# Kernel tuning notes

Hardware: AMD Instinct MI355X
Metric: run time of the kernel (lower is better)

Reference implementation:

```python
import jax, jax.numpy as jnp
import numpy as np

N, M, D, C = 8192, 4096, 512, 100


def mish(x):
    return x * jnp.tanh(jax.nn.softplus(x))


def encode_dml(x, W1, b1, W2, b2):
    # two Linear(d_in, d_in) layers each followed by Mish
    h = mish(x @ W1 + b1)
    return mish(h @ W2 + b2)


def setup_inputs() -> dict:
    key = jax.random.key(0)
    ks = jax.random.split(key, 8)
    s = 1.0 / np.sqrt(D)
    x = jax.random.normal(ks[0], (N, D), dtype=jnp.float32)
    samples = jax.random.normal(ks[1], (M, D), dtype=jnp.float32)
    W1 = jax.random.normal(ks[2], (D, D), dtype=jnp.float32) * s
    b1 = jnp.zeros((D,), dtype=jnp.float32)
    W2 = jax.random.normal(ks[3], (D, D), dtype=jnp.float32) * s
    b2 = jnp.zeros((D,), dtype=jnp.float32)
    Wp = jax.random.normal(ks[4], (M, C), dtype=jnp.float32) * (1.0 / np.sqrt(M))
    bp = jnp.zeros((C,), dtype=jnp.float32)
    return {"x": x, "samples": samples, "W1": W1, "b1": b1,
            "W2": W2, "b2": b2, "Wp": Wp, "bp": bp}


def reference(x, samples, W1, b1, W2, b2, Wp, bp):
    xe = encode_dml(x, W1, b1, W2, b2)        # [N, D]
    se = encode_dml(samples, W1, b1, W2, b2)  # [M, D]
    # Euclidean distance to every anchor, GEMM-trick form of
    # torch.norm(x[:,None,:] - s[None,:,:], dim=-1)
    d2 = (jnp.sum(xe * xe, axis=1)[:, None]
          + jnp.sum(se * se, axis=1)[None, :]
          - 2.0 * (xe @ se.T))                # [N, M]
    dist = jnp.sqrt(jnp.maximum(d2, 0.0))
    z = jnp.tanh(dist @ Wp + bp)              # [N, C]
    return jax.nn.log_softmax(z, axis=1)
```

## Files before the change

### kernel.cpp

```cpp
#include <hip/hip_runtime.h>
#include <hip/hip_bf16.h>
#include <math.h>

#define N_ 8192
#define M_ 4096
#define R_ 12288
#define D_ 512
#define C_ 100
#define CP_ 112
#define NSPLIT_ 8
#define MTILES_ ((M_ / NSPLIT_) / 128)

typedef _Float16 f16;
typedef f16  f16x8 __attribute__((ext_vector_type(8)));
typedef f16  f16x4 __attribute__((ext_vector_type(4)));
typedef float f32x4 __attribute__((ext_vector_type(4)));

__device__ __forceinline__ float mishf(float v) {
    float sp = fmaxf(v, 0.f) + log1pf(expf(-fabsf(v)));
    return v * tanhf(sp);
}

__global__ void prep_all(const float* __restrict__ W1, const float* __restrict__ W2,
                         const float* __restrict__ Wp,
                         f16* __restrict__ w1t, f16* __restrict__ w2t,
                         f16* __restrict__ wpT) {
    __shared__ char pshm[57856];
    const int bid = blockIdx.x, t = threadIdx.x;
    if (bid < 128) {
        float (*ls)[68] = (float (*)[68])pshm;
        const float* W = (bid < 64) ? W1 : W2;
        f16* WT = (bid < 64) ? w1t : w2t;
        int tile = bid & 63;
        int k0 = (tile >> 3) * 64, c0 = (tile & 7) * 64;
        int r = t >> 4, c4 = (t & 15) * 4;
        #pragma unroll
        for (int l = 0; l < 4; ++l) {
            int row = r + 16 * l;
            float4 v = *reinterpret_cast<const float4*>(&W[(size_t)(k0 + row) * D_ + c0 + c4]);
            ls[row][c4 + 0] = v.x; ls[row][c4 + 1] = v.y;
            ls[row][c4 + 2] = v.z; ls[row][c4 + 3] = v.w;
        }
        __syncthreads();
        #pragma unroll
        for (int l = 0; l < 4; ++l) {
            int c = r + 16 * l;
            f16x4 o;
            #pragma unroll
            for (int j = 0; j < 4; ++j) o[j] = (f16)ls[c4 + j][c];
            *reinterpret_cast<f16x4*>(&WT[(size_t)(c0 + c) * D_ + k0 + c4]) = o;
        }
    } else {
        float (*lp)[113] = (float (*)[113])pshm;
        int b = bid - 128;
        int m0 = b * 128;
        for (int id = t; id < 128 * C_; id += 256) {
            int mm = id / C_, c = id - mm * C_;
            lp[mm][c] = Wp[(size_t)(m0 + mm) * C_ + c];
        }
        for (int id = t; id < 128 * (CP_ - C_); id += 256) {
            int mm = id / (CP_ - C_), c = C_ + id % (CP_ - C_);
            lp[mm][c] = 0.f;
        }
        __syncthreads();
        for (int id = t; id < CP_ * 128; id += 256) {
            int c = id >> 7, mm = id & 127;
            wpT[(size_t)c * M_ + m0 + mm] = (f16)lp[mm][c];
        }
    }
}

template<bool NORMS, bool F32IN>
__global__ __launch_bounds__(256) void enc_mfma(
        const void* __restrict__ A1, const void* __restrict__ A2,
        const f16* __restrict__ WT,
        const float* __restrict__ b, f16* __restrict__ out,
        float* __restrict__ np8) {
    __shared__ char smem[24576];
    char* xs = smem;
    char* ws = smem + 8192;
    char* os = smem;

    const int t = threadIdx.x;
    const int lane = t & 63;
    const int w  = t >> 6;
    const int wr = w >> 1, wc = w & 1;
    const int lr = lane & 15, lk = lane >> 4;
    const int c0 = blockIdx.x * 128;
    const int n0 = blockIdx.y * 64;

    const int srow = t >> 3;
    const int sj   = t & 7;
    const int csA  = sj ^ (srow & 7);
    const float* Af = nullptr;
    const f16*   Ah = nullptr;
    size_t gA0;
    if constexpr (F32IN) {
        int roff = (n0 < N_) ? n0 : (n0 - N_);
        Af = (const float*)((n0 < N_) ? A1 : A2);
        gA0 = (size_t)(roff + srow) * D_ + csA * 8;
    } else {
        Ah = (const f16*)A1;
        gA0 = (size_t)(n0 + srow) * D_ + csA * 8;
    }
    const size_t gW0 = (size_t)(c0 + srow) * D_ + csA * 8;
    char* lA = xs + t * 16;
    char* lW = ws + t * 16;

    f16x8 ra[2], rw[4];
    f32x4 acc[2][4];
    #pragma unroll
    for (int i = 0; i < 2; ++i)
        #pragma unroll
        for (int j = 0; j < 4; ++j) acc[i][j] = (f32x4){0.f, 0.f, 0.f, 0.f};

    auto loadA = [&](int p, int kn) -> f16x8 {
        if constexpr (F32IN) {
            float4 u0 = *(const float4*)(Af + gA0 + (size_t)p * 32 * D_ + kn);
            float4 u1 = *(const float4*)(Af + gA0 + (size_t)p * 32 * D_ + kn + 4);
            f16x8 o;
            o[0] = (f16)u0.x; o[1] = (f16)u0.y; o[2] = (f16)u0.z; o[3] = (f16)u0.w;
            o[4] = (f16)u1.x; o[5] = (f16)u1.y; o[6] = (f16)u1.z; o[7] = (f16)u1.w;
            return o;
        } else {
            return *(const f16x8*)(Ah + gA0 + (size_t)p * 32 * D_ + kn);
        }
    };

    #pragma unroll
    for (int p = 0; p < 2; ++p) ra[p] = loadA(p, 0);
    #pragma unroll
    for (int p = 0; p < 4; ++p) rw[p] = *(const f16x8*)(WT + gW0 + (size_t)p * 32 * D_);

    for (int kc = 0; kc < 8; ++kc) {
        __syncthreads();
        #pragma unroll
        for (int p = 0; p < 2; ++p) *(f16x8*)(lA + p * 4096) = ra[p];
        #pragma unroll
        for (int p = 0; p < 4; ++p) *(f16x8*)(lW + p * 4096) = rw[p];
        if (kc < 7) {
            int kn = (kc + 1) * 64;
            #pragma unroll
            for (int p = 0; p < 2; ++p) ra[p] = loadA(p, kn);
            #pragma unroll
            for (int p = 0; p < 4; ++p) rw[p] = *(const f16x8*)(WT + gW0 + (size_t)p * 32 * D_ + kn);
        }
        __syncthreads();
        #pragma unroll
        for (int ks = 0; ks < 2; ++ks) {
            const int csw = (ks * 4 + lk) ^ (lr & 7);
            f16x8 af[2], bf[4];
            #pragma unroll
            for (int i = 0; i < 2; ++i)
                af[i] = *(const f16x8*)(xs + (wr * 32 + i * 16 + lr) * 128 + csw * 16);
            #pragma unroll
            for (int j = 0; j < 4; ++j)
                bf[j] = *(const f16x8*)(ws + (wc * 64 + j * 16 + lr) * 128 + csw * 16);
            #pragma unroll
            for (int i = 0; i < 2; ++i)
                #pragma unroll
                for (int j = 0; j < 4; ++j)
                    acc[i][j] = __builtin_amdgcn_mfma_f32_16x16x32_f16(af[i], bf[j], acc[i][j], 0, 0, 0);
        }
    }
    __syncthreads();
    {
        float bv[4];
        #pragma unroll
        for (int j = 0; j < 4; ++j) bv[j] = b[c0 + wc * 64 + j * 16 + lr];
        float rn[2][4] = {};
        #pragma unroll
        for (int i = 0; i < 2; ++i)
            #pragma unroll
            for (int j = 0; j < 4; ++j)
                #pragma unroll
                for (int q = 0; q < 4; ++q) {
                    float v = mishf(acc[i][j][q] + bv[j]);
                    f16 h = (f16)v;
                    int row_l = wr * 32 + i * 16 + lk * 4 + q;
                    int col_l = wc * 64 + j * 16 + lr;
                    *(f16*)(os + row_l * 256 + (((col_l >> 3) ^ (row_l & 7)) * 16) + (col_l & 7) * 2) = h;
                    if (NORMS) { float fv = (float)h; rn[i][q] = fmaf(fv, fv, rn[i][q]); }
                }
        if (NORMS) {
            #pragma unroll
            for (int i = 0; i < 2; ++i)
                #pragma unroll
                for (int q = 0; q < 4; ++q) {
                    float s = rn[i][q];
                    s += __shfl_xor(s, 1, 64); s += __shfl_xor(s, 2, 64);
                    s += __shfl_xor(s, 4, 64); s += __shfl_xor(s, 8, 64);
                    if (lr == 0)
                        np8[(size_t)(blockIdx.x * 2 + wc) * R_ + n0 + wr * 32 + i * 16 + lk * 4 + q] = s;
                }
        }
    }
    __syncthreads();
    #pragma unroll
    for (int l2 = 0; l2 < 4; ++l2) {
        int id = t + l2 * 256;
        int row = id >> 4, cc = id & 15;
        f16x8 v = *(const f16x8*)(os + row * 256 + ((cc ^ (row & 7)) * 16));
        *(f16x8*)(out + (size_t)(n0 + row) * D_ + c0 + cc * 8) = v;
    }
}

__global__ void np_reduce(const float* __restrict__ np8, float* __restrict__ n2) {
    int id = blockIdx.x * 256 + threadIdx.x;
    float s = 0.f;
    #pragma unroll
    for (int p = 0; p < 8; ++p) s += np8[(size_t)p * R_ + id];
    n2[id] = s;
}

#define LDA3 72
#define LDD3 136
__global__ __launch_bounds__(256, 2) void fused_mfma(
        const f16* __restrict__ xe, const f16* __restrict__ se,
        const float* __restrict__ xn2, const float* __restrict__ sn2,
        const f16* __restrict__ WpT, float* __restrict__ zpart) {
    __shared__ char smem[72192];
    f16*   xs = (f16*)smem;
    f16*   ss = (f16*)(smem + 18432);
    f16*   wp = (f16*)smem;
    f16*   ds = (f16*)(smem + 36864);
    float* xn = (float*)(smem + 71680);

    const int t    = threadIdx.x;
    const int lane = t & 63;
    const int w    = t >> 6;
    const int wr   = w >> 1, wc = w & 1;
    const int lr   = lane & 15, lk = lane >> 4;

    const int n0    = blockIdx.x * 128;
    const int mbase = blockIdx.y * (M_ / NSPLIT_);

    if (t < 128) xn[t] = xn2[n0 + t];

    f32x4 zacc[2][7];
    #pragma unroll
    for (int i = 0; i < 2; ++i)
        #pragma unroll
        for (int j = 0; j < 7; ++j)
            zacc[i][j] = (f32x4){0.f, 0.f, 0.f, 0.f};

    for (int mt = 0; mt < MTILES_; ++mt) {
        const int m0 = mbase + mt * 128;
        f32x4 sacc[4][4];
        #pragma unroll
        for (int i = 0; i < 4; ++i)
            #pragma unroll
            for (int j = 0; j < 4; ++j)
                sacc[i][j] = (f32x4){0.f, 0.f, 0.f, 0.f};

        for (int kc = 0; kc < 8; ++kc) {
            __syncthreads();
            {
                int r = t >> 3, ko = (t & 7) * 8;
                int kg = kc * 64 + ko;
                #pragma unroll
                for (int l = 0; l < 4; ++l) {
                    int row = r + 32 * l;
                    *reinterpret_cast<f16x8*>(&xs[row * LDA3 + ko]) =
                        *reinterpret_cast<const f16x8*>(&xe[(size_t)(n0 + row) * D_ + kg]);
                    *reinterpret_cast<f16x8*>(&ss[row * LDA3 + ko]) =
                        *reinterpret_cast<const f16x8*>(&se[(size_t)(m0 + row) * D_ + kg]);
                }
            }
            __syncthreads();
            #pragma unroll
            for (int ks = 0; ks < 2; ++ks) {
                f16x8 af[4], bf[4];
                #pragma unroll
                for (int i = 0; i < 4; ++i) {
                    af[i] = *reinterpret_cast<const f16x8*>(&xs[(wr * 64 + i * 16 + lr) * LDA3 + ks * 32 + lk * 8]);
                    bf[i] = *reinterpret_cast<const f16x8*>(&ss[(wc * 64 + i * 16 + lr) * LDA3 + ks * 32 + lk * 8]);
                }
                #pragma unroll
                for (int i = 0; i < 4; ++i)
                    #pragma unroll
                    for (int j = 0; j < 4; ++j)
                        sacc[i][j] = __builtin_amdgcn_mfma_f32_16x16x32_f16(af[i], bf[j], sacc[i][j], 0, 0, 0);
            }
        }
        {
            float snr[4];
            #pragma unroll
            for (int j = 0; j < 4; ++j) snr[j] = sn2[m0 + wc * 64 + j * 16 + lr];
            #pragma unroll
            for (int i = 0; i < 4; ++i) {
                #pragma unroll
                for (int j = 0; j < 4; ++j) {
                    #pragma unroll
                    for (int q = 0; q < 4; ++q) {
                        int row_l = wr * 64 + i * 16 + lk * 4 + q;
                        int col_l = wc * 64 + j * 16 + lr;
                        float d2 = xn[row_l] + snr[j] - 2.f * sacc[i][j][q];
                        ds[row_l * LDD3 + col_l] = (f16)sqrtf(fmaxf(d2, 0.f));
                    }
                }
            }
        }
        __syncthreads();
        #pragma unroll
        for (int l = 0; l < 7; ++l) {
            int id = t + l * 256;
            int c = id >> 4, mo = (id & 15) * 8;
            *reinterpret_cast<f16x8*>(&wp[c * LDD3 + mo]) =
                *reinterpret_cast<const f16x8*>(&WpT[(size_t)c * M_ + m0 + mo]);
        }
        __syncthreads();
        #pragma unroll
        for (int ks = 0; ks < 4; ++ks) {
            f16x8 aF0 = *reinterpret_cast<const f16x8*>(&ds[(w * 32 + 0  + lr) * LDD3 + ks * 32 + lk * 8]);
            f16x8 aF1 = *reinterpret_cast<const f16x8*>(&ds[(w * 32 + 16 + lr) * LDD3 + ks * 32 + lk * 8]);
            #pragma unroll
            for (int cb = 0; cb < 7; ++cb) {
                f16x8 bF = *reinterpret_cast<const f16x8*>(&wp[(cb * 16 + lr) * LDD3 + ks * 32 + lk * 8]);
                zacc[0][cb] = __builtin_amdgcn_mfma_f32_16x16x32_f16(aF0, bF, zacc[0][cb], 0, 0, 0);
                zacc[1][cb] = __builtin_amdgcn_mfma_f32_16x16x32_f16(aF1, bF, zacc[1][cb], 0, 0, 0);
            }
        }
    }
    #pragma unroll
    for (int ar = 0; ar < 2; ++ar) {
        #pragma unroll
        for (int cb = 0; cb < 7; ++cb) {
            #pragma unroll
            for (int q = 0; q < 4; ++q) {
                int row = n0 + w * 32 + ar * 16 + lk * 4 + q;
                int col = cb * 16 + lr;
                zpart[((size_t)blockIdx.y * N_ + row) * CP_ + col] = zacc[ar][cb][q];
            }
        }
    }
}

__global__ void z_epilogue(const float* __restrict__ zpart, const float* __restrict__ bp,
                           float* __restrict__ out) {
    const int w = threadIdx.x >> 6, lane = threadIdx.x & 63;
    const int row = blockIdx.x * 4 + w;
    float z0 = 0.f, z1 = 0.f;
    #pragma unroll
    for (int s = 0; s < NSPLIT_; ++s) {
        const float* zp = &zpart[((size_t)s * N_ + row) * CP_];
        z0 += zp[lane];
        if (lane + 64 < CP_) z1 += zp[lane + 64];
    }
    float t0 = tanhf(z0 + bp[lane]);
    bool  v1 = (lane + 64) < C_;
    float t1 = v1 ? tanhf(z1 + bp[lane + 64]) : -INFINITY;
    float mx = fmaxf(t0, t1);
    #pragma unroll
    for (int m = 1; m < 64; m <<= 1) mx = fmaxf(mx, __shfl_xor(mx, m, 64));
    float se_ = expf(t0 - mx) + (v1 ? expf(t1 - mx) : 0.f);
    #pragma unroll
    for (int m = 1; m < 64; m <<= 1) se_ += __shfl_xor(se_, m, 64);
    float lse = mx + logf(se_);
    out[(size_t)row * C_ + lane] = t0 - lse;
    if (v1) out[(size_t)row * C_ + lane + 64] = t1 - lse;
}

extern "C" void kernel_launch(void* const* d_in, const int* in_sizes, int n_in,
                              void* d_out, int out_size, void* d_ws, size_t ws_size,
                              hipStream_t stream) {
    const float* x       = (const float*)d_in[0];
    const float* samples = (const float*)d_in[1];
    const float* W1      = (const float*)d_in[2];
    const float* b1      = (const float*)d_in[3];
    const float* W2      = (const float*)d_in[4];
    const float* b2      = (const float*)d_in[5];
    const float* Wp      = (const float*)d_in[6];
    const float* bp      = (const float*)d_in[7];
    float* out = (float*)d_out;

    char* p = (char*)d_ws;
    float* zpart = (float*)p;
    f16* h   = (f16*)(p + 12582912);
    f16* w1t = (f16*)(p + 25165824);
    f16* w2t = (f16*)(p + 25690112);
    p += (size_t)NSPLIT_ * N_ * CP_ * 4;
    f16*  ef  = (f16*)p;   p += (size_t)R_ * D_ * 2;
    float* np8 = (float*)p; p += (size_t)8 * R_ * 4;
    float* n2  = (float*)p; p += (size_t)R_ * 4;
    f16*  wpT = (f16*)p;   p += (size_t)CP_ * M_ * 2;

    dim3 blk(256);
    prep_all<<<160, blk, 0, stream>>>(W1, W2, Wp, w1t, w2t, wpT);
    enc_mfma<false, true><<<dim3(4, R_ / 64), blk, 0, stream>>>(x, samples, w1t, b1, h, nullptr);
    enc_mfma<true, false><<<dim3(4, R_ / 64), blk, 0, stream>>>(h, nullptr, w2t, b2, ef, np8);
    np_reduce<<<R_ / 256, blk, 0, stream>>>(np8, n2);
    fused_mfma<<<dim3(N_ / 128, NSPLIT_), blk, 0, stream>>>(ef, ef + (size_t)N_ * D_,
                                                           n2, n2 + N_, wpT, zpart);
    z_epilogue<<<N_ / 4, blk, 0, stream>>>(zpart, bp, out);
}
```

Baseline: 174.5 us.

## Load encoder tiles directly into LDS and reorder fused kernel grid

The encoder GEMM now uses global_load_lds to copy W tiles, and f16 A tiles, straight from global memory into shared memory. This replaces the register-staged prefetch, so the explicit double-buffer overlap for those operands is gone. Separately, the fused distance kernel's grid is transposed so the M-split index varies fastest, meaning consecutive blocks share the same row tile of xe. The aim is fewer VGPRs and better cache locality, at the cost of the load latency no longer being hidden behind the previous chunk's MFMAs.

Result: slower. 180.4 us (+3.3%).

```diff
diff --git a/kernel.cpp b/kernel.cpp
--- a/kernel.cpp
+++ b/kernel.cpp
@@ -19,6 +19,12 @@
 __device__ __forceinline__ float mishf(float v) {
     float sp = fmaxf(v, 0.f) + log1pf(expf(-fabsf(v)));
     return v * tanhf(sp);
+}
+
+__device__ __forceinline__ void gll16(const void* g, void* l) {
+    __builtin_amdgcn_global_load_lds(
+        (const __attribute__((address_space(1))) unsigned int*)g,
+        (__attribute__((address_space(3))) unsigned int*)l, 16, 0, 0);
 }
 
 __global__ void prep_all(const float* __restrict__ W1, const float* __restrict__ W2,
@@ -107,7 +113,7 @@
     char* lA = xs + t * 16;
     char* lW = ws + t * 16;
 
-    f16x8 ra[2], rw[4];
+    f16x8 ra[2];
     f32x4 acc[2][4];
     #pragma unroll
     for (int i = 0; i < 2; ++i)
@@ -115,35 +121,36 @@
         for (int j = 0; j < 4; ++j) acc[i][j] = (f32x4){0.f, 0.f, 0.f, 0.f};
 
     auto loadA = [&](int p, int kn) -> f16x8 {
+        float4 u0 = *(const float4*)(Af + gA0 + (size_t)p * 32 * D_ + kn);
+        float4 u1 = *(const float4*)(Af + gA0 + (size_t)p * 32 * D_ + kn + 4);
+        f16x8 o;
+        o[0] = (f16)u0.x; o[1] = (f16)u0.y; o[2] = (f16)u0.z; o[3] = (f16)u0.w;
+        o[4] = (f16)u1.x; o[5] = (f16)u1.y; o[6] = (f16)u1.z; o[7] = (f16)u1.w;
+        return o;
+    };
+
+    if constexpr (F32IN) {
+        #pragma unroll
+        for (int p = 0; p < 2; ++p) ra[p] = loadA(p, 0);
+    }
+
+    for (int kc = 0; kc < 8; ++kc) {
+        __syncthreads();
+        const int kn = kc * 64;
         if constexpr (F32IN) {
-            float4 u0 = *(const float4*)(Af + gA0 + (size_t)p * 32 * D_ + kn);
-            float4 u1 = *(const float4*)(Af + gA0 + (size_t)p * 32 * D_ + kn + 4);
-            f16x8 o;
-            o[0] = (f16)u0.x; o[1] = (f16)u0.y; o[2] = (f16)u0.z; o[3] = (f16)u0.w;
-            o[4] = (f16)u1.x; o[5] = (f16)u1.y; o[6] = (f16)u1.z; o[7] = (f16)u1.w;
-            return o;
+            #pragma unroll
+            for (int p = 0; p < 2; ++p) *(f16x8*)(lA + p * 4096) = ra[p];
         } else {
-            return *(const f16x8*)(Ah + gA0 + (size_t)p * 32 * D_ + kn);
-        }
-    };
-
-    #pragma unroll
-    for (int p = 0; p < 2; ++p) ra[p] = loadA(p, 0);
-    #pragma unroll
-    for (int p = 0; p < 4; ++p) rw[p] = *(const f16x8*)(WT + gW0 + (size_t)p * 32 * D_);
-
-    for (int kc = 0; kc < 8; ++kc) {
-        __syncthreads();
-        #pragma unroll
-        for (int p = 0; p < 2; ++p) *(f16x8*)(lA + p * 4096) = ra[p];
-        #pragma unroll
-        for (int p = 0; p < 4; ++p) *(f16x8*)(lW + p * 4096) = rw[p];
-        if (kc < 7) {
-            int kn = (kc + 1) * 64;
-            #pragma unroll
-            for (int p = 0; p < 2; ++p) ra[p] = loadA(p, kn);
-            #pragma unroll
-            for (int p = 0; p < 4; ++p) rw[p] = *(const f16x8*)(WT + gW0 + (size_t)p * 32 * D_ + kn);
+            #pragma unroll
+            for (int p = 0; p < 2; ++p)
+                gll16(Ah + gA0 + (size_t)p * 32 * D_ + kn, lA + p * 4096);
+        }
+        #pragma unroll
+        for (int p = 0; p < 4; ++p)
+            gll16(WT + gW0 + (size_t)p * 32 * D_ + kn, lW + p * 4096);
+        if (F32IN && kc < 7) {
+            #pragma unroll
+            for (int p = 0; p < 2; ++p) ra[p] = loadA(p, kn + 64);
         }
         __syncthreads();
         #pragma unroll
@@ -232,8 +239,9 @@
     const int wr   = w >> 1, wc = w & 1;
     const int lr   = lane & 15, lk = lane >> 4;
 
-    const int n0    = blockIdx.x * 128;
-    const int mbase = blockIdx.y * (M_ / NSPLIT_);
+    const int n0    = blockIdx.y * 128;
+    const int split = blockIdx.x;
+    const int mbase = split * (M_ / NSPLIT_);
 
     if (t < 128) xn[t] = xn2[n0 + t];
 
@@ -330,7 +338,7 @@
             for (int q = 0; q < 4; ++q) {
                 int row = n0 + w * 32 + ar * 16 + lk * 4 + q;
                 int col = cb * 16 + lr;
-                zpart[((size_t)blockIdx.y * N_ + row) * CP_ + col] = zacc[ar][cb][q];
+                zpart[((size_t)split * N_ + row) * CP_ + col] = zacc[ar][cb][q];
             }
         }
     }
@@ -390,7 +398,7 @@
     enc_mfma<false, true><<<dim3(4, R_ / 64), blk, 0, stream>>>(x, samples, w1t, b1, h, nullptr);
     enc_mfma<true, false><<<dim3(4, R_ / 64), blk, 0, stream>>>(h, nullptr, w2t, b2, ef, np8);
     np_reduce<<<R_ / 256, blk, 0, stream>>>(np8, n2);
-    fused_mfma<<<dim3(N_ / 128, NSPLIT_), blk, 0, stream>>>(ef, ef + (size_t)N_ * D_,
+    fused_mfma<<<dim3(NSPLIT_, N_ / 128), blk, 0, stream>>>(ef, ef + (size_t)N_ * D_,
                                                            n2, n2 + N_, wpT, zpart);
     z_epilogue<<<N_ / 4, blk, 0, stream>>>(zpart, bp, out);
 }
```
